# Performance work log

Hardware: AMD Instinct MI355X
Metric: run time of the kernel (lower is better)

## Reference

```python
import jax, jax.numpy as jnp
import numpy as np

B, L, D, H, E = 32, 100, 128, 8, 64
C = D // H
NEG_SLOPE = 0.2
MASK_VAL = -1e9
LN_EPS = 1e-5


def _glorot(key, shape):
    fan_in, fan_out = shape[-1], shape[-2]
    std = np.sqrt(6.0 / (fan_in + fan_out))
    return jax.random.uniform(key, shape, jnp.float32, -std, std)


def setup_inputs() -> dict:
    key = jax.random.key(0)
    ks = jax.random.split(key, 12)
    x = jax.random.normal(ks[0], (B, L, D), jnp.float32)
    adj = jax.random.randint(ks[1], (B, L, L), 0, 2, jnp.int32)
    e = jax.random.normal(ks[2], (B, L, L, E), jnp.float32)
    Wx = _glorot(ks[3], (D, D))          # linear_x weight (out, in)
    We = _glorot(ks[4], (D, E))          # linear_e weight (out, in)
    att_src = _glorot(ks[5], (H, C))
    att_dst = _glorot(ks[6], (H, C))
    att_e = _glorot(ks[7], (H, C))
    ffn_w = _glorot(ks[8], (D, D))
    ffn_b = jnp.zeros((D,), jnp.float32)
    ln_g = jnp.ones((D,), jnp.float32)
    ln_b = jnp.zeros((D,), jnp.float32)
    return dict(x=x, adj=adj, e=e, Wx=Wx, We=We, att_src=att_src,
                att_dst=att_dst, att_e=att_e, ffn_w=ffn_w, ffn_b=ffn_b,
                ln_g=ln_g, ln_b=ln_b)


def reference(x, adj, e, Wx, We, att_src, att_dst, att_e, ffn_w, ffn_b, ln_g, ln_b):
    Bb, Ll, Dd = x.shape
    Hh, Cc = att_src.shape
    # node / edge projections
    xp = (x @ Wx.T).reshape(Bb, Ll, Hh, Cc)                      # (B,L,H,C)
    ep = jnp.einsum('bije,de->bijd', e, We).reshape(Bb, Ll, Ll, Hh, Cc)  # (B,L,L,H,C)
    # per-head attention logits
    xj = jnp.einsum('blhc,hc->blh', xp, att_src)                 # source score
    xi = jnp.einsum('blhc,hc->blh', xp, att_dst)                 # dest score
    es = jnp.einsum('bijhc,hc->bijh', ep, att_e)                 # edge score
    s = xi[:, :, None, :] + xj[:, None, :, :] + es               # (B,L,L,H)
    s = jax.nn.leaky_relu(s, NEG_SLOPE)
    s = jnp.where((adj != 0)[..., None], s, MASK_VAL)
    alpha = jax.nn.softmax(s, axis=2)                            # softmax over j
    # aggregation: out[b,i,h,c] = sum_j alpha[b,i,j,h] * xp[b,j,h,c]
    out = jnp.einsum('bijh,bjhc->bihc', alpha, xp).reshape(Bb, Ll, Dd)
    # FFN: linear -> layernorm -> relu (dropout p=0)
    h = out @ ffn_w.T + ffn_b
    mu = h.mean(-1, keepdims=True)
    var = jnp.mean((h - mu) ** 2, axis=-1, keepdims=True)
    h = (h - mu) * jax.lax.rsqrt(var + LN_EPS) * ln_g + ln_b
    return jax.nn.relu(h)
```

## Files before the change

### kernel.cpp

```cpp
#include <hip/hip_runtime.h>
#include <hip/hip_bf16.h>

#define NB 32
#define NL 100
#define ND 128
#define NH 8
#define NE 64
#define NC 16

#define WS_XI    0
#define WS_XJ    25600
#define WS_XPBF  51200
#define WS_WFTBF 256000
#define WS_ES    264192
#define WS_TOT   (264192 + NB * NL * NL * NH)

__device__ float g_ws[WS_TOT];

static __device__ __forceinline__ ushort f2bf(float f) {
    union { float f; unsigned u; } v; v.f = f;
    unsigned u = v.u + 0x7FFFu + ((v.u >> 16) & 1u);
    return (ushort)(u >> 16);
}
static __device__ __forceinline__ float bf2f(ushort s) {
    union { unsigned u; float f; } v; v.u = ((unsigned)s) << 16;
    return v.f;
}
static __device__ __forceinline__ float pick8(const float* a, int c) {
    return (c < 4)
        ? ((c < 2) ? (c == 0 ? a[0] : a[1]) : (c == 2 ? a[2] : a[3]))
        : ((c < 6) ? (c == 4 ? a[4] : a[5]) : (c == 6 ? a[6] : a[7]));
}

__global__ __launch_bounds__(256) void mega_kernel(
        const float* __restrict__ x, const float* __restrict__ e,
        const float* __restrict__ Wx, const float* __restrict__ We,
        const float* __restrict__ att_src, const float* __restrict__ att_dst,
        const float* __restrict__ att_e, const float* __restrict__ ffn_w) {
    __shared__ float smem[2048];
    int blk = blockIdx.x;
    int t = threadIdx.x;

    if (blk < 2048) {
        float* projL = smem;
        for (int pid = t; pid < 512; pid += 256) {
            int h = pid >> 6, eix = pid & 63;
            float acc = 0.f;
            #pragma unroll
            for (int c = 0; c < NC; ++c)
                acc += att_e[h * NC + c] * We[(h * NC + c) * NE + eix];
            projL[pid] = acc;
        }
        __syncthreads();
        int lane = t & 63;
        int j_sub = lane >> 3, c_sub = lane & 7;
        const float4* projL4 = (const float4*)projL;
        float4 p4[16];
        #pragma unroll
        for (int h = 0; h < 8; ++h) {
            p4[h * 2]     = projL4[h * 16 + c_sub * 2];
            p4[h * 2 + 1] = projL4[h * 16 + c_sub * 2 + 1];
        }
        const float4* e4 = (const float4*)e;
        int wid = blk * 4 + (t >> 6);
        const int NCHUNK = NB * NL * NL / 8;
        for (int chunk = wid; chunk < NCHUNK; chunk += 2048 * 4) {
            int rid = chunk * 8 + j_sub;
            float4 ev0 = e4[rid * 16 + c_sub * 2];
            float4 ev1 = e4[rid * 16 + c_sub * 2 + 1];
            float part[8];
            #pragma unroll
            for (int h = 0; h < 8; ++h) {
                float4 a = p4[h * 2], bq = p4[h * 2 + 1];
                part[h] = ev0.x * a.x + ev0.y * a.y + ev0.z * a.z + ev0.w * a.w
                        + ev1.x * bq.x + ev1.y * bq.y + ev1.z * bq.z + ev1.w * bq.w;
            }
            #pragma unroll
            for (int st = 1; st < 8; st <<= 1)
                #pragma unroll
                for (int h = 0; h < 8; ++h)
                    part[h] += __shfl_xor(part[h], st);
            g_ws[WS_ES + rid * 8 + c_sub] = pick8(part, c_sub);
        }
    } else if (blk < 2448) {
        int bl0 = (blk - 2048) * 8;
        float* xrowL = smem;
        float* xpL   = smem + 1024;
        const float4* x4 = (const float4*)(x + bl0 * 128);
        float4* xr4 = (float4*)xrowL;
        xr4[t] = x4[t];
        __syncthreads();
        int lane = t & 63, w = t >> 6;
        int d_sub = lane >> 3, c_sub = lane & 7;
        const float4* Wx4 = (const float4*)Wx;
        ushort* xpbf = (ushort*)(g_ws + WS_XPBF);
        #pragma unroll
        for (int rr = 0; rr < 4; ++rr) {
            int d = rr * 32 + w * 8 + d_sub;
            float4 wc0 = Wx4[d * 32 + c_sub * 4 + 0];
            float4 wc1 = Wx4[d * 32 + c_sub * 4 + 1];
            float4 wc2 = Wx4[d * 32 + c_sub * 4 + 2];
            float4 wc3 = Wx4[d * 32 + c_sub * 4 + 3];
            float accs[8];
            #pragma unroll
            for (int r = 0; r < 8; ++r) {
                const float4* xr = (const float4*)(xrowL + r * 128);
                float4 a0 = xr[c_sub * 4 + 0], a1 = xr[c_sub * 4 + 1];
                float4 a2 = xr[c_sub * 4 + 2], a3 = xr[c_sub * 4 + 3];
                accs[r] = wc0.x * a0.x + wc0.y * a0.y + wc0.z * a0.z + wc0.w * a0.w
                        + wc1.x * a1.x + wc1.y * a1.y + wc1.z * a1.z + wc1.w * a1.w
                        + wc2.x * a2.x + wc2.y * a2.y + wc2.z * a2.z + wc2.w * a2.w
                        + wc3.x * a3.x + wc3.y * a3.y + wc3.z * a3.z + wc3.w * a3.w;
            }
            #pragma unroll
            for (int st = 1; st < 8; st <<= 1)
                #pragma unroll
                for (int r = 0; r < 8; ++r)
                    accs[r] += __shfl_xor(accs[r], st);
            float v = pick8(accs, c_sub);
            xpL[c_sub * 128 + d] = v;
            xpbf[(bl0 + c_sub) * 128 + d] = f2bf(v);
        }
        __syncthreads();
        {
            int r = t >> 5, sub = t & 31;
            int h = sub >> 2;
            float sp = 0.f, sd = 0.f;
            #pragma unroll
            for (int q = 0; q < 4; ++q) {
                float xv = xpL[r * 128 + sub * 4 + q];
                sp += xv * att_src[sub * 4 + q];
                sd += xv * att_dst[sub * 4 + q];
            }
            sp += __shfl_xor(sp, 1); sp += __shfl_xor(sp, 2);
            sd += __shfl_xor(sd, 1); sd += __shfl_xor(sd, 2);
            if ((sub & 3) == 0) {
                g_ws[WS_XJ + (bl0 + r) * 8 + h] = sp;
                g_ws[WS_XI + (bl0 + r) * 8 + h] = sd;
            }
        }
    } else {
        int r0 = (blk - 2448) * 8;
        float* tileL = smem;
        int k = t & 127, rh = t >> 7;
        #pragma unroll
        for (int ri = 0; ri < 4; ++ri) {
            int rr = ri * 2 + rh;
            tileL[rr * 128 + k] = ffn_w[(r0 + rr) * 128 + k];
        }
        __syncthreads();
        if (t < 128) {
            ushort* wft = (ushort*)(g_ws + WS_WFTBF);
            unsigned w0 = f2bf(tileL[0 * 128 + t]) | ((unsigned)f2bf(tileL[1 * 128 + t]) << 16);
            unsigned w1 = f2bf(tileL[2 * 128 + t]) | ((unsigned)f2bf(tileL[3 * 128 + t]) << 16);
            unsigned w2 = f2bf(tileL[4 * 128 + t]) | ((unsigned)f2bf(tileL[5 * 128 + t]) << 16);
            unsigned w3 = f2bf(tileL[6 * 128 + t]) | ((unsigned)f2bf(tileL[7 * 128 + t]) << 16);
            uint4 pack; pack.x = w0; pack.y = w1; pack.z = w2; pack.w = w3;
            *(uint4*)(wft + t * 128 + r0) = pack;
        }
    }
}

__global__ __launch_bounds__(256) void gat_main(
        const int* __restrict__ adj, const float* __restrict__ ffn_b,
        const float* __restrict__ ln_g, const float* __restrict__ ln_b,
        float* __restrict__ out) {
    __shared__ ushort xpL[NL * 128];
    __shared__ float s_lds[4][NL * 9];
    __shared__ float partL[2][4][128];
    __shared__ float rowL[4][128];
    __shared__ float hvalL[4][128];
    __shared__ float inv[4][8];
    __shared__ float mr[4][2];

    int blk = blockIdx.x;
    int b = blk / 25, ig = blk % 25;
    int i0 = ig * 4;
    int t = threadIdx.x;

    {
        const uint4* src = (const uint4*)((const ushort*)(g_ws + WS_XPBF) + b * NL * 128);
        uint4* dst = (uint4*)xpL;
        for (int idx = t; idx < NL * 128 / 8; idx += 256)
            dst[idx] = src[idx];
    }
    {
        int h = t & 7, jj = t >> 3;
        #pragma unroll
        for (int ii = 0; ii < 4; ++ii) {
            int bi = b * NL + i0 + ii;
            float xiv = g_ws[WS_XI + bi * 8 + h];
            #pragma unroll
            for (int r = 0; r < 4; ++r) {
                int j = jj + r * 32;
                if (j < NL) {
                    float s = xiv + g_ws[WS_XJ + (b * NL + j) * 8 + h]
                            + g_ws[WS_ES + (bi * NL + j) * 8 + h];
                    s = s > 0.f ? s : 0.2f * s;
                    s = adj[bi * NL + j] ? s : -1e9f;
                    s_lds[ii][j * 9 + h] = s;
                }
            }
        }
    }
    __syncthreads();
    {
        int h = t >> 5, jt = t & 31;
        const float LOG2E = 1.44269504f;
        #pragma unroll
        for (int ii = 0; ii < 4; ++ii) {
            float* sl = s_lds[ii];
            float v0 = sl[jt * 9 + h];
            float v1 = sl[(jt + 32) * 9 + h];
            float v2 = sl[(jt + 64) * 9 + h];
            float v3 = (jt < 4) ? sl[(jt + 96) * 9 + h] : -3.0e38f;
            float m = fmaxf(fmaxf(v0, v1), fmaxf(v2, v3));
            #pragma unroll
            for (int st = 1; st < 32; st <<= 1) m = fmaxf(m, __shfl_xor(m, st));
            float p0 = exp2f((v0 - m) * LOG2E);
            float p1 = exp2f((v1 - m) * LOG2E);
            float p2 = exp2f((v2 - m) * LOG2E);
            float p3 = (jt < 4) ? exp2f((v3 - m) * LOG2E) : 0.f;
            float sum = p0 + p1 + p2 + p3;
            #pragma unroll
            for (int st = 1; st < 32; st <<= 1) sum += __shfl_xor(sum, st);
            sl[jt * 9 + h] = p0;
            sl[(jt + 32) * 9 + h] = p1;
            sl[(jt + 64) * 9 + h] = p2;
            if (jt < 4) sl[(jt + 96) * 9 + h] = p3;
            if (jt == 0) inv[ii][h] = 1.0f / sum;
        }
    }
    __syncthreads();
    {
        int d = t & 127, half = t >> 7, hh = d >> 4;
        float a0 = 0.f, a1 = 0.f, a2 = 0.f, a3 = 0.f;
        int j0 = half * 50;
        #pragma unroll 5
        for (int k = 0; k < 50; ++k) {
            int j = j0 + k;
            float xv = bf2f(xpL[j * 128 + d]);
            a0 = fmaf(s_lds[0][j * 9 + hh], xv, a0);
            a1 = fmaf(s_lds[1][j * 9 + hh], xv, a1);
            a2 = fmaf(s_lds[2][j * 9 + hh], xv, a2);
            a3 = fmaf(s_lds[3][j * 9 + hh], xv, a3);
        }
        partL[half][0][d] = a0; partL[half][1][d] = a1;
        partL[half][2][d] = a2; partL[half][3][d] = a3;
    }
    __syncthreads();
    {
        int d = t & 127, g2 = t >> 7;
        #pragma unroll
        for (int g = 0; g < 2; ++g) {
            int ii = g2 * 2 + g;
            rowL[ii][d] = (partL[0][ii][d] + partL[1][ii][d]) * inv[ii][d >> 4];
        }
    }
    __syncthreads();
    {
        int d = t & 127, half = t >> 7;
        const ushort* wft = (const ushort*)(g_ws + WS_WFTBF);
        float a0 = 0.f, a1 = 0.f, a2 = 0.f, a3 = 0.f;
        int k0 = half * 64;
        #pragma unroll 8
        for (int k = k0; k < k0 + 64; ++k) {
            float wv = bf2f(wft[k * 128 + d]);
            a0 = fmaf(wv, rowL[0][k], a0);
            a1 = fmaf(wv, rowL[1][k], a1);
            a2 = fmaf(wv, rowL[2][k], a2);
            a3 = fmaf(wv, rowL[3][k], a3);
        }
        partL[half][0][d] = a0; partL[half][1][d] = a1;
        partL[half][2][d] = a2; partL[half][3][d] = a3;
    }
    __syncthreads();
    {
        int d = t & 127, g2 = t >> 7;
        float fb = ffn_b[d];
        #pragma unroll
        for (int g = 0; g < 2; ++g) {
            int ii = g2 * 2 + g;
            hvalL[ii][d] = partL[0][ii][d] + partL[1][ii][d] + fb;
        }
    }
    __syncthreads();
    {
        int wv = t >> 6, lane = t & 63;
        float a = hvalL[wv][lane], b2 = hvalL[wv][lane + 64];
        float s1 = a + b2, s2 = a * a + b2 * b2;
        #pragma unroll
        for (int st = 1; st < 64; st <<= 1) {
            s1 += __shfl_xor(s1, st);
            s2 += __shfl_xor(s2, st);
        }
        if (lane == 0) {
            float mu = s1 * (1.0f / 128.0f);
            float var = s2 * (1.0f / 128.0f) - mu * mu;
            mr[wv][0] = mu;
            mr[wv][1] = rsqrtf(var + 1e-5f);
        }
    }
    __syncthreads();
    {
        int d = t & 127, g2 = t >> 7;
        float lg = ln_g[d], lb = ln_b[d];
        #pragma unroll
        for (int g = 0; g < 2; ++g) {
            int ii = g2 * 2 + g;
            float y = (hvalL[ii][d] - mr[ii][0]) * mr[ii][1] * lg + lb;
            out[(b * NL + i0 + ii) * 128 + d] = fmaxf(y, 0.f);
        }
    }
}

extern "C" void kernel_launch(void* const* d_in, const int* in_sizes, int n_in,
                              void* d_out, int out_size, void* d_ws, size_t ws_size,
                              hipStream_t stream) {
    const float* x       = (const float*)d_in[0];
    const int*   adj     = (const int*)  d_in[1];
    const float* e       = (const float*)d_in[2];
    const float* Wx      = (const float*)d_in[3];
    const float* We      = (const float*)d_in[4];
    const float* att_src = (const float*)d_in[5];
    const float* att_dst = (const float*)d_in[6];
    const float* att_e   = (const float*)d_in[7];
    const float* ffn_w   = (const float*)d_in[8];
    const float* ffn_b   = (const float*)d_in[9];
    const float* ln_g    = (const float*)d_in[10];
    const float* ln_b    = (const float*)d_in[11];
    float* out = (float*)d_out;

    hipLaunchKernelGGL(mega_kernel, dim3(2464), dim3(256), 0, stream,
                       x, e, Wx, We, att_src, att_dst, att_e, ffn_w);
    hipLaunchKernelGGL(gat_main, dim3(NB * 25), dim3(256), 0, stream,
                       adj, ffn_b, ln_g, ln_b, out);
}
```

Before: 205.0 us.

## Split fused prep kernel into separate launches and drop bf16 intermediates

Replaces the single heterogeneous mega_kernel with three kernels: weight transpose/projection prep, edge-score reduction, and node projection using a pre-transposed Wx. The main kernel now processes 2 rows per block instead of 4, doubling the grid, and reads fp32 xp directly from global memory instead of staging a bf16 copy in LDS. It removes bf16 rounding of xp and the FFN weight. In exchange it adds two kernel launches, serializes the prep stages, and reloads xp from global memory more times.

```diff
diff --git a/kernel.cpp b/kernel.cpp
--- a/kernel.cpp
+++ b/kernel.cpp
@@ -8,155 +8,111 @@
 #define NE 64
 #define NC 16
 
-#define WS_XI    0
-#define WS_XJ    25600
-#define WS_XPBF  51200
-#define WS_WFTBF 256000
-#define WS_ES    264192
-#define WS_TOT   (264192 + NB * NL * NL * NH)
+#define WS_WXT  0
+#define WS_WFT  16384
+#define WS_PROJ 32768
+#define WS_XI   33280
+#define WS_XJ   58880
+#define WS_XP   84480
+#define WS_ES   (84480 + NB * NL * ND)
+#define WS_TOT  (WS_ES + NB * NL * NL * NH)
 
 __device__ float g_ws[WS_TOT];
 
-static __device__ __forceinline__ ushort f2bf(float f) {
-    union { float f; unsigned u; } v; v.f = f;
-    unsigned u = v.u + 0x7FFFu + ((v.u >> 16) & 1u);
-    return (ushort)(u >> 16);
-}
-static __device__ __forceinline__ float bf2f(ushort s) {
-    union { unsigned u; float f; } v; v.u = ((unsigned)s) << 16;
-    return v.f;
-}
 static __device__ __forceinline__ float pick8(const float* a, int c) {
     return (c < 4)
         ? ((c < 2) ? (c == 0 ? a[0] : a[1]) : (c == 2 ? a[2] : a[3]))
         : ((c < 6) ? (c == 4 ? a[4] : a[5]) : (c == 6 ? a[6] : a[7]));
 }
 
-__global__ __launch_bounds__(256) void mega_kernel(
-        const float* __restrict__ x, const float* __restrict__ e,
+__global__ __launch_bounds__(256) void prep_kernel(
         const float* __restrict__ Wx, const float* __restrict__ We,
-        const float* __restrict__ att_src, const float* __restrict__ att_dst,
         const float* __restrict__ att_e, const float* __restrict__ ffn_w) {
-    __shared__ float smem[2048];
-    int blk = blockIdx.x;
+    int gid = blockIdx.x * 256 + threadIdx.x;
+    if (gid < 16384) {
+        int k = gid >> 7, d = gid & 127;
+        g_ws[WS_WXT + gid] = Wx[d * 128 + k];
+        g_ws[WS_WFT + gid] = ffn_w[d * 128 + k];
+    } else if (gid < 16384 + 512) {
+        int pid = gid - 16384;
+        int h = pid >> 6, eix = pid & 63;
+        float acc = 0.f;
+        #pragma unroll
+        for (int c = 0; c < NC; ++c)
+            acc += att_e[h * NC + c] * We[(h * NC + c) * NE + eix];
+        g_ws[WS_PROJ + pid] = acc;
+    }
+}
+
+__global__ __launch_bounds__(256) void escore_kernel(const float* __restrict__ e) {
+    const float4* proj4 = (const float4*)(g_ws + WS_PROJ);
     int t = threadIdx.x;
-
-    if (blk < 2048) {
-        float* projL = smem;
-        for (int pid = t; pid < 512; pid += 256) {
-            int h = pid >> 6, eix = pid & 63;
-            float acc = 0.f;
-            #pragma unroll
-            for (int c = 0; c < NC; ++c)
-                acc += att_e[h * NC + c] * We[(h * NC + c) * NE + eix];
-            projL[pid] = acc;
-        }
-        __syncthreads();
-        int lane = t & 63;
-        int j_sub = lane >> 3, c_sub = lane & 7;
-        const float4* projL4 = (const float4*)projL;
-        float4 p4[16];
+    int lane = t & 63;
+    int j_sub = lane >> 3, c_sub = lane & 7;
+    float4 p4[16];
+    #pragma unroll
+    for (int h = 0; h < 8; ++h) {
+        p4[h * 2]     = proj4[h * 16 + c_sub * 2];
+        p4[h * 2 + 1] = proj4[h * 16 + c_sub * 2 + 1];
+    }
+    const float4* e4 = (const float4*)e;
+    int wid = blockIdx.x * 4 + (t >> 6);
+    int nw = gridDim.x * 4;
+    for (int chunk = wid; chunk < NB * NL * NL / 8; chunk += nw) {
+        long rid = (long)chunk * 8 + j_sub;
+        float4 ev0 = e4[rid * 16 + c_sub * 2];
+        float4 ev1 = e4[rid * 16 + c_sub * 2 + 1];
+        float part[8];
         #pragma unroll
         for (int h = 0; h < 8; ++h) {
-            p4[h * 2]     = projL4[h * 16 + c_sub * 2];
-            p4[h * 2 + 1] = projL4[h * 16 + c_sub * 2 + 1];
-        }
-        const float4* e4 = (const float4*)e;
-        int wid = blk * 4 + (t >> 6);
-        const int NCHUNK = NB * NL * NL / 8;
-        for (int chunk = wid; chunk < NCHUNK; chunk += 2048 * 4) {
-            int rid = chunk * 8 + j_sub;
-            float4 ev0 = e4[rid * 16 + c_sub * 2];
-            float4 ev1 = e4[rid * 16 + c_sub * 2 + 1];
-            float part[8];
-            #pragma unroll
-            for (int h = 0; h < 8; ++h) {
-                float4 a = p4[h * 2], bq = p4[h * 2 + 1];
-                part[h] = ev0.x * a.x + ev0.y * a.y + ev0.z * a.z + ev0.w * a.w
-                        + ev1.x * bq.x + ev1.y * bq.y + ev1.z * bq.z + ev1.w * bq.w;
-            }
-            #pragma unroll
-            for (int st = 1; st < 8; st <<= 1)
-                #pragma unroll
-                for (int h = 0; h < 8; ++h)
-                    part[h] += __shfl_xor(part[h], st);
-            g_ws[WS_ES + rid * 8 + c_sub] = pick8(part, c_sub);
-        }
-    } else if (blk < 2448) {
-        int bl0 = (blk - 2048) * 8;
-        float* xrowL = smem;
-        float* xpL   = smem + 1024;
-        const float4* x4 = (const float4*)(x + bl0 * 128);
-        float4* xr4 = (float4*)xrowL;
-        xr4[t] = x4[t];
-        __syncthreads();
-        int lane = t & 63, w = t >> 6;
-        int d_sub = lane >> 3, c_sub = lane & 7;
-        const float4* Wx4 = (const float4*)Wx;
-        ushort* xpbf = (ushort*)(g_ws + WS_XPBF);
-        #pragma unroll
-        for (int rr = 0; rr < 4; ++rr) {
-            int d = rr * 32 + w * 8 + d_sub;
-            float4 wc0 = Wx4[d * 32 + c_sub * 4 + 0];
-            float4 wc1 = Wx4[d * 32 + c_sub * 4 + 1];
-            float4 wc2 = Wx4[d * 32 + c_sub * 4 + 2];
-            float4 wc3 = Wx4[d * 32 + c_sub * 4 + 3];
-            float accs[8];
-            #pragma unroll
-            for (int r = 0; r < 8; ++r) {
-                const float4* xr = (const float4*)(xrowL + r * 128);
-                float4 a0 = xr[c_sub * 4 + 0], a1 = xr[c_sub * 4 + 1];
-                float4 a2 = xr[c_sub * 4 + 2], a3 = xr[c_sub * 4 + 3];
-                accs[r] = wc0.x * a0.x + wc0.y * a0.y + wc0.z * a0.z + wc0.w * a0.w
-                        + wc1.x * a1.x + wc1.y * a1.y + wc1.z * a1.z + wc1.w * a1.w
-                        + wc2.x * a2.x + wc2.y * a2.y + wc2.z * a2.z + wc2.w * a2.w
-                        + wc3.x * a3.x + wc3.y * a3.y + wc3.z * a3.z + wc3.w * a3.w;
-            }
-            #pragma unroll
-            for (int st = 1; st < 8; st <<= 1)
-                #pragma unroll
-                for (int r = 0; r < 8; ++r)
-                    accs[r] += __shfl_xor(accs[r], st);
-            float v = pick8(accs, c_sub);
-            xpL[c_sub * 128 + d] = v;
-            xpbf[(bl0 + c_sub) * 128 + d] = f2bf(v);
-        }
-        __syncthreads();
-        {
-            int r = t >> 5, sub = t & 31;
-            int h = sub >> 2;
-            float sp = 0.f, sd = 0.f;
-            #pragma unroll
-            for (int q = 0; q < 4; ++q) {
-                float xv = xpL[r * 128 + sub * 4 + q];
-                sp += xv * att_src[sub * 4 + q];
-                sd += xv * att_dst[sub * 4 + q];
-            }
-            sp += __shfl_xor(sp, 1); sp += __shfl_xor(sp, 2);
-            sd += __shfl_xor(sd, 1); sd += __shfl_xor(sd, 2);
-            if ((sub & 3) == 0) {
-                g_ws[WS_XJ + (bl0 + r) * 8 + h] = sp;
-                g_ws[WS_XI + (bl0 + r) * 8 + h] = sd;
-            }
-        }
-    } else {
-        int r0 = (blk - 2448) * 8;
-        float* tileL = smem;
-        int k = t & 127, rh = t >> 7;
-        #pragma unroll
-        for (int ri = 0; ri < 4; ++ri) {
-            int rr = ri * 2 + rh;
-            tileL[rr * 128 + k] = ffn_w[(r0 + rr) * 128 + k];
-        }
-        __syncthreads();
-        if (t < 128) {
-            ushort* wft = (ushort*)(g_ws + WS_WFTBF);
-            unsigned w0 = f2bf(tileL[0 * 128 + t]) | ((unsigned)f2bf(tileL[1 * 128 + t]) << 16);
-            unsigned w1 = f2bf(tileL[2 * 128 + t]) | ((unsigned)f2bf(tileL[3 * 128 + t]) << 16);
-            unsigned w2 = f2bf(tileL[4 * 128 + t]) | ((unsigned)f2bf(tileL[5 * 128 + t]) << 16);
-            unsigned w3 = f2bf(tileL[6 * 128 + t]) | ((unsigned)f2bf(tileL[7 * 128 + t]) << 16);
-            uint4 pack; pack.x = w0; pack.y = w1; pack.z = w2; pack.w = w3;
-            *(uint4*)(wft + t * 128 + r0) = pack;
+            float4 a = p4[h * 2], bq = p4[h * 2 + 1];
+            part[h] = ev0.x * a.x + ev0.y * a.y + ev0.z * a.z + ev0.w * a.w
+                    + ev1.x * bq.x + ev1.y * bq.y + ev1.z * bq.z + ev1.w * bq.w;
+        }
+        #pragma unroll
+        for (int st = 1; st < 8; st <<= 1)
+            #pragma unroll
+            for (int h = 0; h < 8; ++h)
+                part[h] += __shfl_xor(part[h], st);
+        g_ws[WS_ES + rid * 8 + c_sub] = pick8(part, c_sub);
+    }
+}
+
+__global__ __launch_bounds__(128) void xproj_kernel(
+        const float* __restrict__ x,
+        const float* __restrict__ att_src, const float* __restrict__ att_dst) {
+    __shared__ float xrowL[4][128];
+    int bl0 = blockIdx.x * 4;
+    int t = threadIdx.x;
+    #pragma unroll
+    for (int r = 0; r < 4; ++r)
+        xrowL[r][t] = x[(bl0 + r) * 128 + t];
+    __syncthreads();
+    const float* WxT = g_ws + WS_WXT;
+    float acc0 = 0.f, acc1 = 0.f, acc2 = 0.f, acc3 = 0.f;
+    #pragma unroll 8
+    for (int k = 0; k < 128; ++k) {
+        float wv = WxT[k * 128 + t];
+        acc0 = fmaf(xrowL[0][k], wv, acc0);
+        acc1 = fmaf(xrowL[1][k], wv, acc1);
+        acc2 = fmaf(xrowL[2][k], wv, acc2);
+        acc3 = fmaf(xrowL[3][k], wv, acc3);
+    }
+    float accs[4] = {acc0, acc1, acc2, acc3};
+    float asr = att_src[t], adt = att_dst[t];
+    #pragma unroll
+    for (int r = 0; r < 4; ++r) {
+        g_ws[WS_XP + (bl0 + r) * 128 + t] = accs[r];
+        float sp = accs[r] * asr;
+        float sd = accs[r] * adt;
+        #pragma unroll
+        for (int st = 1; st < 16; st <<= 1) {
+            sp += __shfl_xor(sp, st);
+            sd += __shfl_xor(sd, st);
+        }
+        if ((t & 15) == 0) {
+            g_ws[WS_XJ + (bl0 + r) * 8 + (t >> 4)] = sp;
+            g_ws[WS_XI + (bl0 + r) * 8 + (t >> 4)] = sd;
         }
     }
 }
@@ -165,29 +121,22 @@
         const int* __restrict__ adj, const float* __restrict__ ffn_b,
         const float* __restrict__ ln_g, const float* __restrict__ ln_b,
         float* __restrict__ out) {
-    __shared__ ushort xpL[NL * 128];
-    __shared__ float s_lds[4][NL * 9];
-    __shared__ float partL[2][4][128];
-    __shared__ float rowL[4][128];
-    __shared__ float hvalL[4][128];
-    __shared__ float inv[4][8];
-    __shared__ float mr[4][2];
+    __shared__ float s_lds[2][NL * 9];
+    __shared__ float partL[2][2][128];
+    __shared__ float rowL[2][128];
+    __shared__ float hvalL[2][128];
+    __shared__ float inv[2][8];
+    __shared__ float mr[2][2];
 
     int blk = blockIdx.x;
-    int b = blk / 25, ig = blk % 25;
-    int i0 = ig * 4;
+    int b = blk / 50, i0 = (blk % 50) * 2;
     int t = threadIdx.x;
-
-    {
-        const uint4* src = (const uint4*)((const ushort*)(g_ws + WS_XPBF) + b * NL * 128);
-        uint4* dst = (uint4*)xpL;
-        for (int idx = t; idx < NL * 128 / 8; idx += 256)
-            dst[idx] = src[idx];
-    }
+    const float* xp = g_ws + WS_XP;
+
     {
         int h = t & 7, jj = t >> 3;
         #pragma unroll
-        for (int ii = 0; ii < 4; ++ii) {
+        for (int ii = 0; ii < 2; ++ii) {
             int bi = b * NL + i0 + ii;
             float xiv = g_ws[WS_XI + bi * 8 + h];
             #pragma unroll
@@ -195,7 +144,7 @@
                 int j = jj + r * 32;
                 if (j < NL) {
                     float s = xiv + g_ws[WS_XJ + (b * NL + j) * 8 + h]
-                            + g_ws[WS_ES + (bi * NL + j) * 8 + h];
+                            + g_ws[WS_ES + ((long)bi * NL + j) * 8 + h];
                     s = s > 0.f ? s : 0.2f * s;
                     s = adj[bi * NL + j] ? s : -1e9f;
                     s_lds[ii][j * 9 + h] = s;
@@ -208,7 +157,7 @@
         int h = t >> 5, jt = t & 31;
         const float LOG2E = 1.44269504f;
         #pragma unroll
-        for (int ii = 0; ii < 4; ++ii) {
+        for (int ii = 0; ii < 2; ++ii) {
             float* sl = s_lds[ii];
             float v0 = sl[jt * 9 + h];
             float v1 = sl[(jt + 32) * 9 + h];
@@ -234,83 +183,67 @@
     __syncthreads();
     {
         int d = t & 127, half = t >> 7, hh = d >> 4;
-        float a0 = 0.f, a1 = 0.f, a2 = 0.f, a3 = 0.f;
+        float a0 = 0.f, a1 = 0.f;
         int j0 = half * 50;
         #pragma unroll 5
         for (int k = 0; k < 50; ++k) {
             int j = j0 + k;
-            float xv = bf2f(xpL[j * 128 + d]);
+            float xv = xp[(b * NL + j) * 128 + d];
             a0 = fmaf(s_lds[0][j * 9 + hh], xv, a0);
             a1 = fmaf(s_lds[1][j * 9 + hh], xv, a1);
-            a2 = fmaf(s_lds[2][j * 9 + hh], xv, a2);
-            a3 = fmaf(s_lds[3][j * 9 + hh], xv, a3);
-        }
-        partL[half][0][d] = a0; partL[half][1][d] = a1;
-        partL[half][2][d] = a2; partL[half][3][d] = a3;
-    }
-    __syncthreads();
-    {
-        int d = t & 127, g2 = t >> 7;
-        #pragma unroll
-        for (int g = 0; g < 2; ++g) {
-            int ii = g2 * 2 + g;
-            rowL[ii][d] = (partL[0][ii][d] + partL[1][ii][d]) * inv[ii][d >> 4];
-        }
+        }
+        partL[half][0][d] = a0;
+        partL[half][1][d] = a1;
+    }
+    __syncthreads();
+    {
+        int d = t & 127, ii = t >> 7;
+        rowL[ii][d] = (partL[0][ii][d] + partL[1][ii][d]) * inv[ii][d >> 4];
     }
     __syncthreads();
     {
         int d = t & 127, half = t >> 7;
-        const ushort* wft = (const ushort*)(g_ws + WS_WFTBF);
-        float a0 = 0.f, a1 = 0.f, a2 = 0.f, a3 = 0.f;
+        const float* WfT = g_ws + WS_WFT;
+        float a0 = 0.f, a1 = 0.f;
         int k0 = half * 64;
         #pragma unroll 8
         for (int k = k0; k < k0 + 64; ++k) {
-            float wv = bf2f(wft[k * 128 + d]);
+            float wv = WfT[k * 128 + d];
             a0 = fmaf(wv, rowL[0][k], a0);
             a1 = fmaf(wv, rowL[1][k], a1);
-            a2 = fmaf(wv, rowL[2][k], a2);
-            a3 = fmaf(wv, rowL[3][k], a3);
-        }
-        partL[half][0][d] = a0; partL[half][1][d] = a1;
-        partL[half][2][d] = a2; partL[half][3][d] = a3;
-    }
-    __syncthreads();
-    {
-        int d = t & 127, g2 = t >> 7;
-        float fb = ffn_b[d];
-        #pragma unroll
-        for (int g = 0; g < 2; ++g) {
-            int ii = g2 * 2 + g;
-            hvalL[ii][d] = partL[0][ii][d] + partL[1][ii][d] + fb;
-        }
-    }
-    __syncthreads();
-    {
-        int wv = t >> 6, lane = t & 63;
-        float a = hvalL[wv][lane], b2 = hvalL[wv][lane + 64];
-        float s1 = a + b2, s2 = a * a + b2 * b2;
-        #pragma unroll
-        for (int st = 1; st < 64; st <<= 1) {
-            s1 += __shfl_xor(s1, st);
-            s2 += __shfl_xor(s2, st);
-        }
-        if (lane == 0) {
-            float mu = s1 * (1.0f / 128.0f);
-            float var = s2 * (1.0f / 128.0f) - mu * mu;
-            mr[wv][0] = mu;
-            mr[wv][1] = rsqrtf(var + 1e-5f);
-        }
-    }
-    __syncthreads();
-    {
-        int d = t & 127, g2 = t >> 7;
-        float lg = ln_g[d], lb = ln_b[d];
-        #pragma unroll
-        for (int g = 0; g < 2; ++g) {
-            int ii = g2 * 2 + g;
-            float y = (hvalL[ii][d] - mr[ii][0]) * mr[ii][1] * lg + lb;
-            out[(b * NL + i0 + ii) * 128 + d] = fmaxf(y, 0.f);
-        }
+        }
+        partL[half][0][d] = a0;
+        partL[half][1][d] = a1;
+    }
+    __syncthreads();
+    {
+        int d = t & 127, ii = t >> 7;
+        hvalL[ii][d] = partL[0][ii][d] + partL[1][ii][d] + ffn_b[d];
+    }
+    __syncthreads();
+    {
+        int row = t >> 6, lane = t & 63;
+        if (row < 2) {
+            float a = hvalL[row][lane], b2 = hvalL[row][lane + 64];
+            float s1 = a + b2, s2 = a * a + b2 * b2;
+            #pragma unroll
+            for (int st = 1; st < 64; st <<= 1) {
+                s1 += __shfl_xor(s1, st);
+                s2 += __shfl_xor(s2, st);
+            }
+            if (lane == 0) {
+                float mu = s1 * (1.0f / 128.0f);
+                float var = s2 * (1.0f / 128.0f) - mu * mu;
+                mr[row][0] = mu;
+                mr[row][1] = rsqrtf(var + 1e-5f);
+            }
+        }
+    }
+    __syncthreads();
+    {
+        int d = t & 127, ii = t >> 7;
+        float y = (hvalL[ii][d] - mr[ii][0]) * mr[ii][1] * ln_g[d] + ln_b[d];
+        out[(b * NL + i0 + ii) * 128 + d] = fmaxf(y, 0.f);
     }
 }
 
@@ -331,8 +264,11 @@
     const float* ln_b    = (const float*)d_in[11];
     float* out = (float*)d_out;
 
-    hipLaunchKernelGGL(mega_kernel, dim3(2464), dim3(256), 0, stream,
-                       x, e, Wx, We, att_src, att_dst, att_e, ffn_w);
-    hipLaunchKernelGGL(gat_main, dim3(NB * 25), dim3(256), 0, stream,
+    hipLaunchKernelGGL(prep_kernel, dim3(66), dim3(256), 0, stream,
+                       Wx, We, att_e, ffn_w);
+    hipLaunchKernelGGL(escore_kernel, dim3(2048), dim3(256), 0, stream, e);
+    hipLaunchKernelGGL(xproj_kernel, dim3(NB * NL / 4), dim3(128), 0, stream,
+                       x, att_src, att_dst);
+    hipLaunchKernelGGL(gat_main, dim3(NB * 50), dim3(256), 0, stream,
                        adj, ffn_b, ln_g, ln_b, out);
 }
```

Measured after the change: 188.6 us (median of 2 runs). 8.0% less time.
